# Kernel tuning notes

Measured on AMD Instinct MI355X. Metric: run time of the kernel, lower is better.

Reference implementation:

```python
import jax, jax.numpy as jnp
import numpy as np

DIM = 8      # channels (from CxWxW_Attention(8, 4, False))
HEADS = 4    # num_heads
EPS = 1e-12  # torch F.normalize eps


def setup_inputs() -> dict:
    key = jax.random.key(0)
    k0, k1, k2, k3 = jax.random.split(key, 4)
    b, c, h, w = 16, DIM, 512, 512
    x = jax.random.normal(k0, (b, c, h, w), jnp.float32)
    # 1x1 conv producing qkv (bias=False): weight (3c, c)
    w_qkv = jax.random.normal(k1, (3 * c, c), jnp.float32) * 0.1
    # 3x3 depthwise conv on qkv, groups=3c: weight (3c, 1, 3, 3)
    w_dw = jax.random.normal(k2, (3 * c, 1, 3, 3), jnp.float32) * 0.1
    # 1x1 projection out: weight (c, c)
    w_out = jax.random.normal(k3, (c, c), jnp.float32) * 0.1
    # per-head learned temperature, init ones; broadcasts over (b, head, c, w, w)
    temperature = jnp.ones((HEADS, 1, 1, 1), jnp.float32)
    return dict(x=x, w_qkv=w_qkv, w_dw=w_dw, w_out=w_out, temperature=temperature)


def _dwconv3x3(x, wgt):
    # depthwise 3x3, padding=1, groups = channels
    C = x.shape[1]
    return jax.lax.conv_general_dilated(
        x, wgt, window_strides=(1, 1), padding=((1, 1), (1, 1)),
        dimension_numbers=("NCHW", "OIHW", "NCHW"), feature_group_count=C)


def _l2norm(t):
    # torch.nn.functional.normalize along last dim
    n = jnp.sqrt(jnp.sum(t * t, axis=-1, keepdims=True))
    return t / jnp.maximum(n, EPS)


def reference(x, w_qkv, w_dw, w_out, temperature):
    b, c, h, w = x.shape
    heads, ch = HEADS, c // HEADS
    # qkv = dwconv3x3(conv1x1(x))
    qkv = jnp.einsum("bchw,oc->bohw", x, w_qkv)
    qkv = _dwconv3x3(qkv, w_dw)
    q, k, v = jnp.split(qkv, 3, axis=1)
    # rearrange 'b (head ch) h w -> b head ch w h' : width attends, height = feature
    def split_heads(t):
        return t.reshape(b, heads, ch, h, w).transpose(0, 1, 2, 4, 3)
    q, k, v = split_heads(q), split_heads(k), split_heads(v)
    q = _l2norm(q)
    k = _l2norm(k)
    # attention map of shape (b, head, ch, W, W)  -> the 'C x W x W' attention
    attn = jnp.einsum("bncwh,bncvh->bncwv", q, k) * temperature
    attn = jax.nn.softmax(attn, axis=-1)
    out = jnp.einsum("bncwv,bncvh->bncwh", attn, v)  # (b, head, ch, w, h)
    # rearrange back 'b head ch w h -> b (head ch) h w'
    out = out.transpose(0, 1, 2, 4, 3).reshape(b, c, h, w)
    return jnp.einsum("bchw,oc->bohw", out, w_out)
```

## Files before the change

kernel.cpp:

```cpp
#include <hip/hip_runtime.h>
#include <hip/hip_bf16.h>

typedef __attribute__((ext_vector_type(4))) float f32x4;
typedef __attribute__((ext_vector_type(2))) float f32x2;
typedef __attribute__((ext_vector_type(8))) short s16x8;
typedef __attribute__((ext_vector_type(4))) short s16x4;
typedef __attribute__((ext_vector_type(4))) unsigned short u16x4;

#define HW 512
#define NSLICE 128

__global__ __launch_bounds__(256) void qkv_fused(
    const float* __restrict__ x, const float* __restrict__ wqkv,
    const float* __restrict__ wdw,
    __hip_bfloat16* __restrict__ qT, __hip_bfloat16* __restrict__ kT,
    __hip_bfloat16* __restrict__ vS,
    float* __restrict__ qss, float* __restrict__ kss)
{
  const int b = blockIdx.y;
  const int tile = blockIdx.x;
  const int h0 = (tile >> 4) * 32;
  const int w0 = (tile & 15) * 32;
  const int tid = threadIdx.x;

  __shared__ float ts[4][1156][2];
  __shared__ __hip_bfloat16 ot[8][32][36];
  __shared__ float colsq[4][8][32];
  __shared__ float wq_s[24][8];
  __shared__ float wd_s[24][12];

  if (tid < 192) wq_s[tid >> 3][tid & 7] = wqkv[tid];
  if (tid < 216) wd_s[tid / 9][tid % 9] = wdw[tid];

  float xr[5][8];
  #pragma unroll
  for (int p = 0; p < 5; ++p) {
    int i = tid + p * 256;
    if (i < 1156) {
      int ih = h0 - 1 + i / 34, iw = w0 - 1 + i % 34;
      bool ok = (ih >= 0 && ih < HW && iw >= 0 && iw < HW);
      #pragma unroll
      for (int c = 0; c < 8; ++c) {
        xr[p][c] = ok ? x[((size_t)(b * 8 + c) * HW + ih) * HW + iw] : 0.f;
      }
    }
  }
  __syncthreads();

  const int tw = tid & 31;
  const int th = tid >> 5;
  const int lane = tid & 63;
  const int wv = tid >> 6;

  #pragma unroll
  for (int g = 0; g < 3; ++g) {
    #pragma unroll
    for (int p = 0; p < 5; ++p) {
      int i = tid + p * 256;
      if (i < 1156) {
        #pragma unroll
        for (int op = 0; op < 4; ++op) {
          const int o = g * 8 + op * 2;
          float a0 = 0.f, a1 = 0.f;
          #pragma unroll
          for (int c = 0; c < 8; ++c) {
            a0 += xr[p][c] * wq_s[o][c];
            a1 += xr[p][c] * wq_s[o + 1][c];
          }
          ts[op][i][0] = a0;
          ts[op][i][1] = a1;
        }
      }
    }
    __syncthreads();

    #pragma unroll
    for (int op = 0; op < 4; ++op) {
      const int o = g * 8 + op * 2;
      float w2[6][3][2];
      #pragma unroll
      for (int r = 0; r < 6; ++r)
        #pragma unroll
        for (int c = 0; c < 3; ++c) {
          f32x2 v = *(const f32x2*)&ts[op][(4 * th + r) * 34 + tw + c][0];
          w2[r][c][0] = v[0];
          w2[r][c][1] = v[1];
        }
      float o0[4], o1[4];
      #pragma unroll
      for (int r = 0; r < 4; ++r) { o0[r] = 0.f; o1[r] = 0.f; }
      #pragma unroll
      for (int di = 0; di < 3; ++di)
        #pragma unroll
        for (int dj = 0; dj < 3; ++dj) {
          const float wd0 = wd_s[o][di * 3 + dj];
          const float wd1 = wd_s[o + 1][di * 3 + dj];
          #pragma unroll
          for (int r = 0; r < 4; ++r) {
            o0[r] += w2[r + di][dj][0] * wd0;
            o1[r] += w2[r + di][dj][1] * wd1;
          }
        }
      if (g < 2) {
        float s0 = o0[0] * o0[0] + o0[1] * o0[1] + o0[2] * o0[2] + o0[3] * o0[3];
        float s1 = o1[0] * o1[0] + o1[1] * o1[1] + o1[2] * o1[2] + o1[3] * o1[3];
        s0 += __shfl_xor(s0, 32);
        s1 += __shfl_xor(s1, 32);
        if (lane < 32) {
          colsq[wv][op * 2][tw] = s0;
          colsq[wv][op * 2 + 1][tw] = s1;
        }
        #pragma unroll
        for (int r = 0; r < 4; ++r) {
          ot[op * 2][tw][4 * th + r] = __float2bfloat16(o0[r]);
          ot[op * 2 + 1][tw][4 * th + r] = __float2bfloat16(o1[r]);
        }
      } else {
        #pragma unroll
        for (int r = 0; r < 4; ++r) {
          ot[op * 2][4 * th + r][tw] = __float2bfloat16(o0[r]);
          ot[op * 2 + 1][4 * th + r][tw] = __float2bfloat16(o1[r]);
        }
      }
    }
    __syncthreads();

    {
      const int rr = tid >> 3, cc = tid & 7;
      #pragma unroll
      for (int o = 0; o < 8; ++o) {
        s16x4 v = *(const s16x4*)&ot[o][rr][cc * 4];
        const size_t sb = (size_t)(b * 8 + o) * HW * HW;
        if (g == 0) {
          *(s16x4*)(qT + sb + (size_t)(h0 >> 5) * HW * 32 + (size_t)(w0 + rr) * 32 + cc * 4) = v;
        } else if (g == 1) {
          *(s16x4*)(kT + sb + (size_t)(h0 >> 5) * HW * 32 + (size_t)(w0 + rr) * 32 + cc * 4) = v;
        } else {
          *(s16x4*)(vS + sb + (size_t)(w0 >> 5) * HW * 32 + (size_t)(h0 + rr) * 32 + cc * 4) = v;
        }
      }
    }
    if (g < 2) {
      const int o = tid >> 5, w = tid & 31;
      float s = colsq[0][o][w] + colsq[1][o][w] + colsq[2][o][w] + colsq[3][o][w];
      float* dst = (g == 0 ? qss : kss) + (size_t)(b * 8 + o) * HW + w0 + w;
      atomicAdd(dst, s);
    }
  }
}

#define LDS_P    0
#define OFF_RMAX 65536
#define OFF_RSUM 67584
#define OFF_RMAXF 69632
#define OFF_RSINV 69888
#define OFF_SQ   70144
#define OFF_SK   70400
#define ATTN_LDS_SIZE 72448

#define GL4(D, VOFF, BASE) \
  asm volatile("global_load_dwordx4 %0, %1, %2 offset:0"    : "=v"(D[0]) : "v"(VOFF), "s"(BASE)); \
  asm volatile("global_load_dwordx4 %0, %1, %2 offset:1024" : "=v"(D[1]) : "v"(VOFF), "s"(BASE)); \
  asm volatile("global_load_dwordx4 %0, %1, %2 offset:2048" : "=v"(D[2]) : "v"(VOFF), "s"(BASE)); \
  asm volatile("global_load_dwordx4 %0, %1, %2 offset:3072" : "=v"(D[3]) : "v"(VOFF), "s"(BASE));

#define LOADSET1(AF, BF, CHN) { \
  const char* bq_ = qs + (size_t)(CHN) * 32768; \
  const char* bk_ = ks + (size_t)(CHN) * 32768; \
  GL4(AF, voffQ, bq_) \
  GL4(BF, voffK, bk_) }

#define LOADSETV(VF, CHN) { \
  const char* bv_ = vs + (size_t)(CHN) * 32768; \
  GL4(VF, voffK, bv_) }

#define WAITV(N) \
  asm volatile("s_waitcnt vmcnt(" #N ")"); \
  __builtin_amdgcn_sched_barrier(0);

#define LOADP(AF, S) { \
    const int cbp_ = (S) * 64 + klo; \
    _Pragma("unroll") for (int m_ = 0; m_ < 4; ++m_) { \
      const int row_ = m_ * 16 + arow; \
      AF[m_] = *(const s16x8*)(ldsP + row_ * 1024 + (cbp_ ^ ((row_ & 7) << 4))); } }
#define MFMA16(AF, BF, ACC) { \
    _Pragma("unroll") for (int m_ = 0; m_ < 4; ++m_) \
      _Pragma("unroll") for (int n_ = 0; n_ < 4; ++n_) \
        ACC[m_][n_] = __builtin_amdgcn_mfma_f32_16x16x32_bf16(AF[m_], BF[n_], ACC[m_][n_], 0, 0, 0); }

__global__ __launch_bounds__(512, 1) void attn_kernel(
    const __hip_bfloat16* __restrict__ qT, const __hip_bfloat16* __restrict__ kT,
    const __hip_bfloat16* __restrict__ vS, __hip_bfloat16* __restrict__ Obuf,
    const float* __restrict__ qss, const float* __restrict__ kss,
    const float* __restrict__ temp)
{
  extern __shared__ char smem[];
  char* ldsP = smem + LDS_P;
  float* red_max  = (float*)(smem + OFF_RMAX);
  float* red_sum  = (float*)(smem + OFF_RSUM);
  float* red_maxf = (float*)(smem + OFF_RMAXF);
  float* rsinv    = (float*)(smem + OFF_RSINV);
  float* sq_l     = (float*)(smem + OFF_SQ);
  float* sk_l     = (float*)(smem + OFF_SK);

  const int tid = threadIdx.x;
  const int lane = tid & 63;
  const int wv = tid >> 6;
  const int p = blockIdx.x;
  const int slice = (p & 7) + 8 * (p >> 6);
  const int rblk = (p >> 3) & 7;
  const int w0 = rblk * 64;
  const size_t sbase = (size_t)slice * HW * HW;
  const char* qs = (const char*)(qT + sbase);
  const char* ks = (const char*)(kT + sbase);
  const char* vs = (const char*)(vS + sbase);

  const int klo = (lane >> 4) << 4;
  const int arow = lane & 15;
  const int voffQ = (w0 + arow) * 64 + klo;
  const int voffK = (wv * 64 + arow) * 64 + klo;

  f32x4 acc[4][4];
  #pragma unroll
  for (int m = 0; m < 4; ++m)
    #pragma unroll
    for (int n = 0; n < 4; ++n) acc[m][n] = (f32x4){0.f, 0.f, 0.f, 0.f};

  const float tmp = temp[(slice & 7) >> 1];
  if (tid < 64) sq_l[tid] = tmp / fmaxf(sqrtf(qss[(size_t)slice * HW + w0 + tid]), 1e-12f);
  sk_l[tid] = 1.f / fmaxf(sqrtf(kss[(size_t)slice * HW + tid]), 1e-12f);
  __builtin_amdgcn_sched_barrier(0);

  s16x8 afA[4], bfA[4], afB[4], bfB[4], afC[4], bfC[4], afD[4], bfD[4];
  LOADSET1(afA, bfA, 0)
  LOADSET1(afB, bfB, 1)
  LOADSET1(afC, bfC, 2)
  LOADSET1(afD, bfD, 3)

  #pragma unroll
  for (int g = 0; g < 3; ++g) {
    WAITV(24) MFMA16(afA, bfA, acc) LOADSET1(afA, bfA, 4 * g + 4)
    WAITV(24) MFMA16(afB, bfB, acc) LOADSET1(afB, bfB, 4 * g + 5)
    WAITV(24) MFMA16(afC, bfC, acc) LOADSET1(afC, bfC, 4 * g + 6)
    WAITV(24) MFMA16(afD, bfD, acc) LOADSET1(afD, bfD, 4 * g + 7)
  }
  WAITV(24) MFMA16(afA, bfA, acc)
  WAITV(16) MFMA16(afB, bfB, acc)
  WAITV(8)  MFMA16(afC, bfC, acc)
  WAITV(0)  MFMA16(afD, bfD, acc)
  __syncthreads();

  float srow[4][4], scol[4];
  #pragma unroll
  for (int m = 0; m < 4; ++m)
    #pragma unroll
    for (int r = 0; r < 4; ++r)
      srow[m][r] = sq_l[m * 16 + ((lane >> 4) << 2) + r];
  #pragma unroll
  for (int n = 0; n < 4; ++n) scol[n] = sk_l[wv * 64 + n * 16 + (lane & 15)];

  float rmax[4][4];
  #pragma unroll
  for (int m = 0; m < 4; ++m)
    #pragma unroll
    for (int r = 0; r < 4; ++r) {
      float mx = -1e30f;
      #pragma unroll
      for (int n = 0; n < 4; ++n) {
        float v = acc[m][n][r] * srow[m][r] * scol[n];
        acc[m][n][r] = v;
        mx = fmaxf(mx, v);
      }
      mx = fmaxf(mx, __shfl_xor(mx, 1));
      mx = fmaxf(mx, __shfl_xor(mx, 2));
      mx = fmaxf(mx, __shfl_xor(mx, 4));
      mx = fmaxf(mx, __shfl_xor(mx, 8));
      rmax[m][r] = mx;
    }
  if ((lane & 15) == 0) {
    #pragma unroll
    for (int m = 0; m < 4; ++m)
      #pragma unroll
      for (int r = 0; r < 4; ++r)
        red_max[(m * 16 + ((lane >> 4) << 2) + r) * 8 + wv] = rmax[m][r];
  }
  __syncthreads();
  if (tid < 64) {
    float mx = red_max[tid * 8];
    #pragma unroll
    for (int g = 1; g < 8; ++g) mx = fmaxf(mx, red_max[tid * 8 + g]);
    red_maxf[tid] = mx;
  }
  __syncthreads();

  float gmax[4][4];
  #pragma unroll
  for (int m = 0; m < 4; ++m)
    #pragma unroll
    for (int r = 0; r < 4; ++r)
      gmax[m][r] = red_maxf[m * 16 + ((lane >> 4) << 2) + r];

  s16x8 vfA[4], vfB[4], vfC[4], vfD[4];
  LOADSETV(vfA, 0)
  LOADSETV(vfB, 1)
  LOADSETV(vfC, 2)
  LOADSETV(vfD, 3)

  float rs[4][4];
  #pragma unroll
  for (int m = 0; m < 4; ++m)
    #pragma unroll
    for (int r = 0; r < 4; ++r) rs[m][r] = 0.f;
  #pragma unroll
  for (int m = 0; m < 4; ++m)
    #pragma unroll
    for (int n = 0; n < 4; ++n)
      #pragma unroll
      for (int r = 0; r < 4; ++r) {
        int row = m * 16 + ((lane >> 4) << 2) + r;
        int col = wv * 64 + n * 16 + (lane & 15);
        float pv = __expf(acc[m][n][r] - gmax[m][r]);
        rs[m][r] += pv;
        *(__hip_bfloat16*)(ldsP + row * 1024 + ((col * 2) ^ ((row & 7) << 4))) =
            __float2bfloat16(pv);
      }
  #pragma unroll
  for (int m = 0; m < 4; ++m)
    #pragma unroll
    for (int r = 0; r < 4; ++r) {
      float s = rs[m][r];
      s += __shfl_xor(s, 1);
      s += __shfl_xor(s, 2);
      s += __shfl_xor(s, 4);
      s += __shfl_xor(s, 8);
      if ((lane & 15) == 0)
        red_sum[(m * 16 + ((lane >> 4) << 2) + r) * 8 + wv] = s;
    }
  __syncthreads();
  if (tid < 64) {
    float s = 0.f;
    #pragma unroll
    for (int g = 0; g < 8; ++g) s += red_sum[tid * 8 + g];
    rsinv[tid] = 1.f / s;
  }

  f32x4 acc2[4][4];
  #pragma unroll
  for (int m = 0; m < 4; ++m)
    #pragma unroll
    for (int n = 0; n < 4; ++n) acc2[m][n] = (f32x4){0.f, 0.f, 0.f, 0.f};

  #pragma unroll
  for (int g = 0; g < 3; ++g) {
    WAITV(12) { s16x8 pf[4]; LOADP(pf, 4 * g + 0) MFMA16(pf, vfA, acc2) } LOADSETV(vfA, 4 * g + 4)
    WAITV(12) { s16x8 pf[4]; LOADP(pf, 4 * g + 1) MFMA16(pf, vfB, acc2) } LOADSETV(vfB, 4 * g + 5)
    WAITV(12) { s16x8 pf[4]; LOADP(pf, 4 * g + 2) MFMA16(pf, vfC, acc2) } LOADSETV(vfC, 4 * g + 6)
    WAITV(12) { s16x8 pf[4]; LOADP(pf, 4 * g + 3) MFMA16(pf, vfD, acc2) } LOADSETV(vfD, 4 * g + 7)
  }
  WAITV(12) { s16x8 pf[4]; LOADP(pf, 12) MFMA16(pf, vfA, acc2) }
  WAITV(8)  { s16x8 pf[4]; LOADP(pf, 13) MFMA16(pf, vfB, acc2) }
  WAITV(4)  { s16x8 pf[4]; LOADP(pf, 14) MFMA16(pf, vfC, acc2) }
  WAITV(0)  { s16x8 pf[4]; LOADP(pf, 15) MFMA16(pf, vfD, acc2) }
  __syncthreads();

  float rinv[4][4];
  #pragma unroll
  for (int m = 0; m < 4; ++m)
    #pragma unroll
    for (int r = 0; r < 4; ++r)
      rinv[m][r] = rsinv[m * 16 + ((lane >> 4) << 2) + r];

  char* ldsO = ldsP + wv * 8192;
  #pragma unroll
  for (int m = 0; m < 4; ++m)
    #pragma unroll
    for (int n = 0; n < 4; ++n)
      #pragma unroll
      for (int r = 0; r < 4; ++r) {
        int row = m * 16 + ((lane >> 4) << 2) + r;
        int col = n * 16 + (lane & 15);
        *(__hip_bfloat16*)(ldsO + row * 128 + col * 2) =
            __float2bfloat16(acc2[m][n][r] * rinv[m][r]);
      }
  __syncthreads();
  __hip_bfloat16* ob = Obuf + sbase + (size_t)w0 * HW + wv * 64;
  #pragma unroll
  for (int it = 0; it < 8; ++it) {
    int row = it * 8 + (lane >> 3);
    int c = (lane & 7) << 4;
    s16x8 v = *(const s16x8*)(ldsO + row * 128 + c);
    *(s16x8*)((char*)ob + (size_t)row * 1024 + c) = v;
  }
}

__global__ __launch_bounds__(256) void proj_kernel(
    const __hip_bfloat16* __restrict__ Obuf, const float* __restrict__ wout,
    float* __restrict__ out)
{
  const int b = blockIdx.y;
  const int t = blockIdx.x;
  const int h0 = (t >> 5) * 64;
  const int w0 = (t & 31) * 16;
  const int tid = threadIdx.x;
  __shared__ float os[8][16][65];
  __shared__ float wo_s[64];
  if (tid < 64) wo_s[tid] = wout[tid];
  {
    int r = tid >> 4;
    int c4 = (tid & 15) * 4;
    #pragma unroll
    for (int o = 0; o < 8; ++o) {
      const __hip_bfloat16* p = Obuf + ((size_t)(b * 8 + o) * HW + w0 + r) * HW + h0 + c4;
      u16x4 v = *(const u16x4*)p;
      #pragma unroll
      for (int i = 0; i < 4; ++i)
        os[o][r][c4 + i] = __uint_as_float((unsigned)v[i] << 16);
    }
  }
  __syncthreads();
  const int w = tid & 15;
  #pragma unroll
  for (int ih = 0; ih < 4; ++ih) {
    int h = ih * 16 + (tid >> 4);
    float ov[8];
    #pragma unroll
    for (int o = 0; o < 8; ++o) ov[o] = os[o][w][h];
    #pragma unroll
    for (int jo = 0; jo < 8; ++jo) {
      float a = 0.f;
      #pragma unroll
      for (int o = 0; o < 8; ++o) a += ov[o] * wo_s[jo * 8 + o];
      out[((size_t)(b * 8 + jo) * HW + h0 + h) * HW + w0 + w] = a;
    }
  }
}

extern "C" void kernel_launch(void* const* d_in, const int* in_sizes, int n_in,
                              void* d_out, int out_size, void* d_ws, size_t ws_size,
                              hipStream_t stream) {
  (void)in_sizes; (void)n_in; (void)out_size; (void)ws_size;
  const float* x    = (const float*)d_in[0];
  const float* wqkv = (const float*)d_in[1];
  const float* wdw  = (const float*)d_in[2];
  const float* wout = (const float*)d_in[3];
  const float* temp = (const float*)d_in[4];
  float* out = (float*)d_out;

  char* ws = (char*)d_ws;
  const size_t plane = (size_t)NSLICE * HW * HW * 2;
  __hip_bfloat16* qT = (__hip_bfloat16*)(ws);
  __hip_bfloat16* kT = (__hip_bfloat16*)(ws + plane);
  __hip_bfloat16* vS = (__hip_bfloat16*)(ws + 2 * plane);
  __hip_bfloat16* Ob = (__hip_bfloat16*)(ws + 3 * plane);
  float* qss = (float*)(ws + 4 * plane);
  float* kss = (float*)(ws + 4 * plane + (size_t)NSLICE * HW * 4);

  hipMemsetAsync(qss, 0, 2 * (size_t)NSLICE * HW * 4, stream);
  qkv_fused<<<dim3(256, 16), 256, 0, stream>>>(x, wqkv, wdw, qT, kT, vS, qss, kss);
  hipFuncSetAttribute((const void*)attn_kernel,
                      hipFuncAttributeMaxDynamicSharedMemorySize, ATTN_LDS_SIZE);
  attn_kernel<<<dim3(1024), 512, ATTN_LDS_SIZE, stream>>>(qT, kT, vS, Ob, qss, kss, temp);
  proj_kernel<<<dim3(256, 16), 256, 0, stream>>>(Ob, wout, out);
}
```

Baseline: 341.6 us.

## Stage Q tile in LDS once and stream only K from global

Before, each of the 8 waves reloaded the same 64-row Q tile from global memory for every channel chunk. Now the block loads the Q tile into padded LDS once and each wave reads its A fragments from LDS, so only K stays in the global prefetch pipeline (wait counts adjusted to match). The LDS fragment reads are also issued before the vmcnt wait in both the QK and PV loops so LDS latency overlaps outstanding global loads. The cost is an extra LDS region and padding, a block-wide barrier before the first MFMA, and an up-front Q load that is not overlapped.

```diff
diff --git a/kernel.cpp b/kernel.cpp
--- a/kernel.cpp
+++ b/kernel.cpp
@@ -149,14 +149,15 @@
   }
 }
 
-#define LDS_P    0
-#define OFF_RMAX 65536
-#define OFF_RSUM 67584
-#define OFF_RMAXF 69632
-#define OFF_RSINV 69888
-#define OFF_SQ   70144
-#define OFF_SK   70400
-#define ATTN_LDS_SIZE 72448
+#define QROW 1040
+#define LDS_QP   0
+#define OFF_RMAX 66560
+#define OFF_RSUM 68608
+#define OFF_RMAXF 70656
+#define OFF_RSINV 70912
+#define OFF_SQ   71168
+#define OFF_SK   71424
+#define ATTN_LDS_SIZE 73472
 
 #define GL4(D, VOFF, BASE) \
   asm volatile("global_load_dwordx4 %0, %1, %2 offset:0"    : "=v"(D[0]) : "v"(VOFF), "s"(BASE)); \
@@ -164,10 +165,8 @@
   asm volatile("global_load_dwordx4 %0, %1, %2 offset:2048" : "=v"(D[2]) : "v"(VOFF), "s"(BASE)); \
   asm volatile("global_load_dwordx4 %0, %1, %2 offset:3072" : "=v"(D[3]) : "v"(VOFF), "s"(BASE));
 
-#define LOADSET1(AF, BF, CHN) { \
-  const char* bq_ = qs + (size_t)(CHN) * 32768; \
+#define LOADSETK(BF, CHN) { \
   const char* bk_ = ks + (size_t)(CHN) * 32768; \
-  GL4(AF, voffQ, bq_) \
   GL4(BF, voffK, bk_) }
 
 #define LOADSETV(VF, CHN) { \
@@ -177,6 +176,11 @@
 #define WAITV(N) \
   asm volatile("s_waitcnt vmcnt(" #N ")"); \
   __builtin_amdgcn_sched_barrier(0);
+
+#define LDSQ(QF, S) { \
+    const int cq_ = (S) * 64 + klo; \
+    _Pragma("unroll") for (int m_ = 0; m_ < 4; ++m_) \
+      QF[m_] = *(const s16x8*)(ldsQ + (m_ * 16 + arow) * QROW + cq_); }
 
 #define LOADP(AF, S) { \
     const int cbp_ = (S) * 64 + klo; \
@@ -195,7 +199,8 @@
     const float* __restrict__ temp)
 {
   extern __shared__ char smem[];
-  char* ldsP = smem + LDS_P;
+  char* ldsQ = smem + LDS_QP;
+  char* ldsP = smem + LDS_QP;
   float* red_max  = (float*)(smem + OFF_RMAX);
   float* red_sum  = (float*)(smem + OFF_RSUM);
   float* red_maxf = (float*)(smem + OFF_RMAXF);
@@ -217,37 +222,47 @@
 
   const int klo = (lane >> 4) << 4;
   const int arow = lane & 15;
-  const int voffQ = (w0 + arow) * 64 + klo;
   const int voffK = (wv * 64 + arow) * 64 + klo;
 
-  f32x4 acc[4][4];
-  #pragma unroll
-  for (int m = 0; m < 4; ++m)
-    #pragma unroll
-    for (int n = 0; n < 4; ++n) acc[m][n] = (f32x4){0.f, 0.f, 0.f, 0.f};
-
+  {
+    const int r = tid >> 3;
+    const int seg = tid & 7;
+    #pragma unroll
+    for (int i = 0; i < 8; ++i) {
+      const int chn_i = seg * 2 + (i >> 2);
+      s16x8 v = *(const s16x8*)(qs + (size_t)chn_i * 32768 + (size_t)(w0 + r) * 64 + (i & 3) * 16);
+      *(s16x8*)(ldsQ + r * QROW + seg * 128 + i * 16) = v;
+    }
+  }
   const float tmp = temp[(slice & 7) >> 1];
   if (tid < 64) sq_l[tid] = tmp / fmaxf(sqrtf(qss[(size_t)slice * HW + w0 + tid]), 1e-12f);
   sk_l[tid] = 1.f / fmaxf(sqrtf(kss[(size_t)slice * HW + tid]), 1e-12f);
+  __syncthreads();
+
+  f32x4 acc[4][4];
+  #pragma unroll
+  for (int m = 0; m < 4; ++m)
+    #pragma unroll
+    for (int n = 0; n < 4; ++n) acc[m][n] = (f32x4){0.f, 0.f, 0.f, 0.f};
   __builtin_amdgcn_sched_barrier(0);
 
-  s16x8 afA[4], bfA[4], afB[4], bfB[4], afC[4], bfC[4], afD[4], bfD[4];
-  LOADSET1(afA, bfA, 0)
-  LOADSET1(afB, bfB, 1)
-  LOADSET1(afC, bfC, 2)
-  LOADSET1(afD, bfD, 3)
+  s16x8 bfA[4], bfB[4], bfC[4], bfD[4];
+  LOADSETK(bfA, 0)
+  LOADSETK(bfB, 1)
+  LOADSETK(bfC, 2)
+  LOADSETK(bfD, 3)
 
   #pragma unroll
   for (int g = 0; g < 3; ++g) {
-    WAITV(24) MFMA16(afA, bfA, acc) LOADSET1(afA, bfA, 4 * g + 4)
-    WAITV(24) MFMA16(afB, bfB, acc) LOADSET1(afB, bfB, 4 * g + 5)
-    WAITV(24) MFMA16(afC, bfC, acc) LOADSET1(afC, bfC, 4 * g + 6)
-    WAITV(24) MFMA16(afD, bfD, acc) LOADSET1(afD, bfD, 4 * g + 7)
-  }
-  WAITV(24) MFMA16(afA, bfA, acc)
-  WAITV(16) MFMA16(afB, bfB, acc)
-  WAITV(8)  MFMA16(afC, bfC, acc)
-  WAITV(0)  MFMA16(afD, bfD, acc)
+    { s16x8 qf[4]; LDSQ(qf, 4 * g + 0) WAITV(12) MFMA16(qf, bfA, acc) } LOADSETK(bfA, 4 * g + 4)
+    { s16x8 qf[4]; LDSQ(qf, 4 * g + 1) WAITV(12) MFMA16(qf, bfB, acc) } LOADSETK(bfB, 4 * g + 5)
+    { s16x8 qf[4]; LDSQ(qf, 4 * g + 2) WAITV(12) MFMA16(qf, bfC, acc) } LOADSETK(bfC, 4 * g + 6)
+    { s16x8 qf[4]; LDSQ(qf, 4 * g + 3) WAITV(12) MFMA16(qf, bfD, acc) } LOADSETK(bfD, 4 * g + 7)
+  }
+  { s16x8 qf[4]; LDSQ(qf, 12) WAITV(12) MFMA16(qf, bfA, acc) }
+  { s16x8 qf[4]; LDSQ(qf, 13) WAITV(8)  MFMA16(qf, bfB, acc) }
+  { s16x8 qf[4]; LDSQ(qf, 14) WAITV(4)  MFMA16(qf, bfC, acc) }
+  { s16x8 qf[4]; LDSQ(qf, 15) WAITV(0)  MFMA16(qf, bfD, acc) }
   __syncthreads();
 
   float srow[4][4], scol[4];
@@ -352,15 +367,15 @@
 
   #pragma unroll
   for (int g = 0; g < 3; ++g) {
-    WAITV(12) { s16x8 pf[4]; LOADP(pf, 4 * g + 0) MFMA16(pf, vfA, acc2) } LOADSETV(vfA, 4 * g + 4)
-    WAITV(12) { s16x8 pf[4]; LOADP(pf, 4 * g + 1) MFMA16(pf, vfB, acc2) } LOADSETV(vfB, 4 * g + 5)
-    WAITV(12) { s16x8 pf[4]; LOADP(pf, 4 * g + 2) MFMA16(pf, vfC, acc2) } LOADSETV(vfC, 4 * g + 6)
-    WAITV(12) { s16x8 pf[4]; LOADP(pf, 4 * g + 3) MFMA16(pf, vfD, acc2) } LOADSETV(vfD, 4 * g + 7)
-  }
-  WAITV(12) { s16x8 pf[4]; LOADP(pf, 12) MFMA16(pf, vfA, acc2) }
-  WAITV(8)  { s16x8 pf[4]; LOADP(pf, 13) MFMA16(pf, vfB, acc2) }
-  WAITV(4)  { s16x8 pf[4]; LOADP(pf, 14) MFMA16(pf, vfC, acc2) }
-  WAITV(0)  { s16x8 pf[4]; LOADP(pf, 15) MFMA16(pf, vfD, acc2) }
+    { s16x8 pf[4]; LOADP(pf, 4 * g + 0) WAITV(12) MFMA16(pf, vfA, acc2) } LOADSETV(vfA, 4 * g + 4)
+    { s16x8 pf[4]; LOADP(pf, 4 * g + 1) WAITV(12) MFMA16(pf, vfB, acc2) } LOADSETV(vfB, 4 * g + 5)
+    { s16x8 pf[4]; LOADP(pf, 4 * g + 2) WAITV(12) MFMA16(pf, vfC, acc2) } LOADSETV(vfC, 4 * g + 6)
+    { s16x8 pf[4]; LOADP(pf, 4 * g + 3) WAITV(12) MFMA16(pf, vfD, acc2) } LOADSETV(vfD, 4 * g + 7)
+  }
+  { s16x8 pf[4]; LOADP(pf, 12) WAITV(12) MFMA16(pf, vfA, acc2) }
+  { s16x8 pf[4]; LOADP(pf, 13) WAITV(8)  MFMA16(pf, vfB, acc2) }
+  { s16x8 pf[4]; LOADP(pf, 14) WAITV(4)  MFMA16(pf, vfC, acc2) }
+  { s16x8 pf[4]; LOADP(pf, 15) WAITV(0)  MFMA16(pf, vfD, acc2) }
   __syncthreads();
 
   float rinv[4][4];
```

Result: faster. 323.0 us (-5.5%).
